# Kernel tuning notes

Hardware: AMD Instinct MI355X
Metric: run time of the kernel (lower is better)

## Reference

```python
import jax, jax.numpy as jnp
import numpy as np
import math

B, S, H, W, C = 8, 16, 512, 512, 1
NT, WIN, SIGMA, ITERS = 256, 21, 2.0, 5
K = WIN * WIN

_SOBEL_X = jnp.array([[-1., 0., 1.], [-2., 0., 2.], [-1., 0., 1.]], jnp.float32).reshape(3, 3, 1, 1)
_SOBEL_Y = jnp.array([[-1., -2., -1.], [0., 0., 0.], [1., 2., 1.]], jnp.float32).reshape(3, 3, 1, 1)


def _win_weights():
    c = WIN // 2
    yy, xx = np.mgrid[0:WIN, 0:WIN]
    d = np.sqrt((xx - c) ** 2 + (yy - c) ** 2)
    g = 1.0 / (SIGMA * math.sqrt(2 * math.pi)) * np.exp(-0.5 * (d / SIGMA) ** 2)
    return jnp.asarray(g.reshape(K), dtype=jnp.float32)


def _sampling_grid():
    lin = jnp.linspace(-1.0, 1.0, WIN)
    x_t, y_t = jnp.meshgrid(lin, lin)  # 'xy' indexing, matches tf.meshgrid
    return jnp.stack([x_t.reshape(-1), y_t.reshape(-1)])  # [2, K]


def _bilinear(sampler, frames2):
    # sampler [B,NT,2,K]; frames2 [B,2,H,W] -> samples [B,2,NT,K]
    x = sampler[:, :, 0] * (WIN * 0.5)  # [B,NT,K] pixel coords
    y = sampler[:, :, 1] * (WIN * 0.5)
    x0 = jnp.clip(jnp.floor(x), 0, W - 1)
    x1 = jnp.clip(jnp.floor(x) + 1, 0, W - 1)
    y0 = jnp.clip(jnp.floor(y), 0, H - 1)
    y1 = jnp.clip(jnp.floor(y) + 1, 0, H - 1)
    wa = (y1 - y) * (x1 - x)
    wb = (y1 - y) * (x - x0)
    wc = (y - y0) * (x1 - x)
    wd = (y - y0) * (x - x0)
    flat = frames2.reshape(frames2.shape[0], 2, H * W)

    def gat(yi, xi):
        idx = (yi.astype(jnp.int32) * W + xi.astype(jnp.int32)).reshape(yi.shape[0], 1, -1)
        idx = jnp.broadcast_to(idx, (yi.shape[0], 2, idx.shape[-1]))
        return jnp.take_along_axis(flat, idx, axis=2).reshape(-1, 2, NT, K)

    Ia, Ib, Ic, Id = gat(y0, x0), gat(y0, x1), gat(y1, x0), gat(y1, x1)
    return (wa[:, None] * Ia + wb[:, None] * Ib + wc[:, None] * Ic + wd[:, None] * Id)


def _calc_velocity(first, second, ww):
    # first/second [B,NT,K] windows; LK 2x2 normal-equation solve per track
    img = first.reshape(-1, WIN, WIN, 1)
    dn = ('NHWC', 'HWIO', 'NHWC')
    Ix = jax.lax.conv_general_dilated(img, _SOBEL_X, (1, 1), 'SAME', dimension_numbers=dn).reshape(-1, NT, K)
    Iy = jax.lax.conv_general_dilated(img, _SOBEL_Y, (1, 1), 'SAME', dimension_numbers=dn).reshape(-1, NT, K)
    A = jnp.stack([Ix, Iy], axis=-1)  # [B,NT,K,2]
    ATA = jnp.einsum('bnki,bnkj->bnij', A, A * ww[None, None, :, None])
    a, b = ATA[..., 0, 0], ATA[..., 0, 1]
    c, d = ATA[..., 1, 0], ATA[..., 1, 1]
    inv_det = 1.0 / (a * d - b * c + 1e-7)
    bvec = -(second - first) * ww  # [B,NT,K]
    ATb = jnp.einsum('bnki,bnk->bni', A, bvec)
    vx = inv_det * (d * ATb[..., 0] - b * ATb[..., 1])
    vy = inv_det * (-c * ATb[..., 0] + a * ATb[..., 1])
    return jnp.stack([vx, vy], axis=-1)  # [B,NT,2]


def _iterative_lk(sampler, frames2, ww):
    out = _bilinear(sampler, frames2)
    first = out[:, 0]
    v = _calc_velocity(first, out[:, 1], ww)
    sampler = sampler + v[..., None]
    sum_v = v
    for _ in range(ITERS - 1):
        out = _bilinear(sampler, frames2)
        v = _calc_velocity(first, out[:, 1], ww)
        sampler = sampler + v[..., None]
        sum_v = sum_v + v
    return sampler, sum_v


def setup_inputs() -> dict:
    key = jax.random.key(0)
    k1, k2 = jax.random.split(key)
    track_locs = jax.random.uniform(k1, (B, NT, 2), dtype=jnp.float32)
    imgs = jax.random.uniform(k2, (B, S, H, W, C), dtype=jnp.float32)
    return {"track_locs": track_locs, "imgs": imgs}


def reference(track_locs, imgs):
    imgs2 = imgs[..., 0]  # [B,S,H,W], c==1
    cr = jnp.array([W / WIN, H / WIN], jnp.float32)
    ww = _win_weights()
    init = track_locs.reshape(-1, NT, 2) * cr + cr  # [B,NT,2]
    sampler = init[..., None] + _sampling_grid()[None, None]  # [B,NT,2,K]
    sampler, sv = _iterative_lk(sampler, imgs2[:, 0:2], ww)
    pos0 = init
    pos1 = init + sv
    fa = jnp.moveaxis(imgs2[:, 1:S - 1], 1, 0)  # [S-2,B,H,W]
    fb = jnp.moveaxis(imgs2[:, 2:S], 1, 0)

    def step(carry, x):
        smp, prev = carry
        frames2 = jnp.stack(x, axis=1)  # [B,2,H,W]
        smp, svv = _iterative_lk(smp, frames2, ww)
        pos = prev + svv
        return (smp, pos), pos

    _, poss = jax.lax.scan(step, (sampler, pos1), (fa, fb))
    tot = jnp.concatenate([pos0[None], pos1[None], poss], axis=0)  # [S,B,NT,2]
    tot = jnp.transpose(tot, (1, 2, 0, 3))  # [B,NT,S,2]
    return (tot - cr) / cr
```

## Files before the change

### kernel.cpp

```cpp
#pragma clang fp contract(off)
#include <hip/hip_runtime.h>
#include <math.h>


#define WINSZ 21
#define KPTS  441
#define NPT   7
#define PSTR  452
#define RDIM  24
#define RSTR  25

struct SB {
  float pqT[6][PSTR];
  float fw[23][25];
  float regA[RDIM * RSTR];
  float regB[RDIM * RSTR];
};

__device__ __forceinline__ float bilinf(const float* __restrict__ F,
                                        float x, float y) {
  #pragma clang fp contract(off)
  float fx = floorf(x), fy = floorf(y);
  float x0 = fminf(fmaxf(fx, 0.0f), 511.0f);
  float x1a = fx + 1.0f;
  float x1 = fminf(fmaxf(x1a, 0.0f), 511.0f);
  float y0 = fminf(fmaxf(fy, 0.0f), 511.0f);
  float y1a = fy + 1.0f;
  float y1 = fminf(fmaxf(y1a, 0.0f), 511.0f);
  float dy1 = y1 - y, dx1 = x1 - x, dy0 = y - y0, dx0 = x - x0;
  float wa = dy1 * dx1;
  float wb = dy1 * dx0;
  float wc = dy0 * dx1;
  float wd = dy0 * dx0;
  int jx0 = (int)x0, jx1 = (int)x1, jy0 = (int)y0, jy1 = (int)y1;
  float Ia = F[jy0 * 512 + jx0];
  float Ib = F[jy0 * 512 + jx1];
  float Ic = F[jy1 * 512 + jx0];
  float Id = F[jy1 * 512 + jx1];
  float pA = wa * Ia;
  float pB = wb * Ib;
  float pC = wc * Ic;
  float pD = wd * Id;
  float s = pA + pB;
  s = s + pC;
  s = s + pD;
  return s;
}

__device__ __forceinline__ void wcalc(float x, float y, int cb,
                                      float* w, int* idx) {
  #pragma clang fp contract(off)
  float fx = floorf(x), fy = floorf(y);
  float x1 = fx + 1.0f;
  float y1 = fy + 1.0f;
  float dy1 = y1 - y, dx1 = x1 - x, dy0 = y - fy, dx0 = x - fx;
  w[0] = dy1 * dx1;
  w[1] = dy1 * dx0;
  w[2] = dy0 * dx1;
  w[3] = dy0 * dx0;
  int ix0 = (int)fx, iy0 = (int)fy;
  *idx = iy0 * RSTR + ix0 - cb;
}

__device__ __forceinline__ float rsum(const float* __restrict__ reg,
                                      const float* w, int idx) {
  #pragma clang fp contract(off)
  float Ia = reg[idx];
  float Ib = reg[idx + 1];
  float Ic = reg[idx + RSTR];
  float Id = reg[idx + RSTR + 1];
  float pA = w[0] * Ia;
  float pB = w[1] * Ib;
  float pC = w[2] * Ic;
  float pD = w[3] * Id;
  float s = pA + pB;
  s = s + pC;
  s = s + pD;
  return s;
}

__global__ __launch_bounds__(64) void lk_track(
    const float* __restrict__ track_locs,
    const float* __restrict__ imgs,
    float* __restrict__ out)
{
  #pragma clang fp contract(off)
  __shared__ SB S;
  const float CRF = (float)(512.0 / 21.0);
  const int SS = 16, HW = 512 * 512;

  const int tr   = blockIdx.x;
  const int b    = tr >> 8;
  const int lane = threadIdx.x;

  for (int i = lane; i < 23 * 25; i += 64) (&S.fw[0][0])[i] = 0.0f;

  const bool act = (lane < 63);
  int   rr[NPT], cc[NPT];
  float gxv[NPT], gyv[NPT], wwv[NPT];
  const double gnorm = 1.0 / (2.0 * sqrt(2.0 * 3.141592653589793));
#pragma unroll
  for (int j = 0; j < NPT; j++) {
    int k = lane * NPT + j;
    if (k >= KPTS) k = 0;
    int r = k / WINSZ, c = k % WINSZ;
    rr[j] = r; cc[j] = c;
    gxv[j] = (c == 20) ? 1.0f : (float)((double)c * 0.1 - 1.0);
    gyv[j] = (r == 20) ? 1.0f : (float)((double)r * 0.1 - 1.0);
    double dd = sqrt((double)((c - 10) * (c - 10) + (r - 10) * (r - 10)));
    double q  = dd / 2.0;
    wwv[j] = (float)(gnorm * exp(-0.5 * (q * q)));
  }

  int soff[9], loff[9];
#pragma unroll
  for (int i = 0; i < 9; i++) {
    int f = lane + 64 * i;
    int r = f / RDIM;
    int c = f - RDIM * r;
    soff[i] = r * 512 + c;
    loff[i] = r * RSTR + c;
  }

  const float* tl = track_locs + (size_t)tr * 2;
  float mx = tl[0] * CRF; float initx = mx + CRF;
  float my = tl[1] * CRF; float inity = my + CRF;

  float sx[NPT], sy[NPT];
#pragma unroll
  for (int j = 0; j < NPT; j++) { sx[j] = initx + gxv[j]; sy[j] = inity + gyv[j]; }

  float px = initx, py = inity;
  if (lane == 0) {
    float* o = out + (size_t)tr * SS * 2;
    float n0 = initx - CRF; o[0] = n0 / CRF;
    float n1 = inity - CRF; o[1] = n1 / CRF;
  }

  int g6 = lane >> 3; if (g6 > 5) g6 = g6 - 2;
  const int grp2 = lane >> 5;
  const float* row6 = &S.pqT[g6][0];
  const float* rowB = &S.pqT[4 + grp2][0];

  float fv[NPT], scv[NPT], ixv[NPT], iyv[NPT];

  for (int t = 0; t < SS - 1; t++) {
    const float* F0 = imgs + ((size_t)b * SS + t) * HW;
    const float* F1 = F0 + HW;

    __syncthreads();

    float xmn = sx[0], xmx = sx[0], ymn = sy[0], ymx = sy[0];
#pragma unroll
    for (int j = 1; j < NPT; j++) {
      xmn = fminf(xmn, sx[j]); xmx = fmaxf(xmx, sx[j]);
      ymn = fminf(ymn, sy[j]); ymx = fmaxf(ymx, sy[j]);
    }
#pragma unroll
    for (int m = 32; m >= 1; m >>= 1) {
      xmn = fminf(xmn, __shfl_xor(xmn, m, 64));
      xmx = fmaxf(xmx, __shfl_xor(xmx, m, 64));
      ymn = fminf(ymn, __shfl_xor(ymn, m, 64));
      ymx = fmaxf(ymx, __shfl_xor(ymx, m, 64));
    }
    float xminp = xmn * 10.5f, xmaxp = xmx * 10.5f;
    float yminp = ymn * 10.5f, ymaxp = ymx * 10.5f;
    float bxf = floorf(xminp), byf = floorf(yminp);
    bool fast = (bxf >= 0.0f) && (byf >= 0.0f) &&
                (bxf <= 488.0f) && (byf <= 488.0f) &&
                (xmaxp < bxf + 23.0f) && (ymaxp < byf + 23.0f);
    int gbase = 0, cb = 0;
    if (fast) {
      int bx = (int)bxf, by = (int)byf;
      gbase = by * 512 + bx;
      cb = by * RSTR + bx;
    }

    if (fast) {
#pragma unroll
      for (int i = 0; i < 9; i++) S.regA[loff[i]] = F0[gbase + soff[i]];
#pragma unroll
      for (int i = 0; i < 9; i++) S.regB[loff[i]] = F1[gbase + soff[i]];
      __syncthreads();
#pragma unroll
      for (int j = 0; j < NPT; j++) {
        float x = sx[j] * 10.5f, y = sy[j] * 10.5f;
        float w[4]; int id;
        wcalc(x, y, cb, w, &id);
        fv[j]  = rsum(S.regA, w, id);
        scv[j] = rsum(S.regB, w, id);
        if (act) S.fw[rr[j] + 1][cc[j] + 1] = fv[j];
      }
    } else {
#pragma unroll
      for (int j = 0; j < NPT; j++) {
        float x = sx[j] * 10.5f, y = sy[j] * 10.5f;
        fv[j]  = bilinf(F0, x, y);
        scv[j] = bilinf(F1, x, y);
        if (act) S.fw[rr[j] + 1][cc[j] + 1] = fv[j];
      }
    }
    __syncthreads();

#pragma unroll
    for (int j = 0; j < NPT; j++) {
      int r = rr[j], c = cc[j];
      float a00 = S.fw[r][c],     a01 = S.fw[r][c + 1],     a02 = S.fw[r][c + 2];
      float a10 = S.fw[r + 1][c],                           a12 = S.fw[r + 1][c + 2];
      float a20 = S.fw[r + 2][c], a21 = S.fw[r + 2][c + 1], a22 = S.fw[r + 2][c + 2];
      float xc0 = -a00;
      float xc1 = 2.0f * a12;
      float xc2 = a02 + (-a20);
      float xc3 = -2.0f * a10;
      float xh0 = xc0 + xc1;
      float xh1 = xc2 + xc3;
      float Ix = xh0 + xh1;
      Ix = Ix + a22;
      float yc0 = -a00;
      float yc1 = -2.0f * a01;
      float yc2 = (-a02) + a20;
      float yc3 = 2.0f * a21;
      float yh0 = yc0 + yc1;
      float yh1 = yc2 + yc3;
      float Iy = yh0 + yh1;
      Iy = Iy + a22;
      ixv[j] = Ix; iyv[j] = Iy;
      if (act) {
        int k = lane * NPT + j;
        float tx = Ix * wwv[j];
        float ty = Iy * wwv[j];
        float p0 = Ix * tx;
        float p1 = Ix * ty;
        float p2 = Iy * tx;
        float p3 = Iy * ty;
        S.pqT[0][k] = p0;
        S.pqT[1][k] = p1;
        S.pqT[2][k] = p2;
        S.pqT[3][k] = p3;
        float d2 = fv[j] - scv[j];
        float bw = d2 * wwv[j];
        float u0 = ixv[j] * bw;
        float u1 = iyv[j] * bw;
        S.pqT[4][k] = u0;
        S.pqT[5][k] = u1;
      }
    }
    __syncthreads();

    float acc = 0.f;
#pragma unroll 11
    for (int m = 0; m < 110; m++) {
      float4 v = *reinterpret_cast<const float4*>(&row6[4 * m]);
      acc = acc + v.x;
      acc = acc + v.y;
      acc = acc + v.z;
      acc = acc + v.w;
    }
    acc = acc + row6[440];
    float aa = __shfl(acc, 0,  64);
    float bb = __shfl(acc, 8,  64);
    float cN = __shfl(acc, 16, 64);
    float dN = __shfl(acc, 24, 64);
    float s0 = __shfl(acc, 32, 64);
    float s1 = __shfl(acc, 40, 64);
    float q0 = aa * dN;
    float q1 = bb * cN;
    float det = q0 - q1;
    det = det + 1e-7f;
    float inv_det = 1.0f / det;

    float svx = 0.f, svy = 0.f;
    for (int it = 0; it < 5; it++) {
      if (it > 0) {
        float xmn2 = sx[0], xmx2 = sx[0], ymn2 = sy[0], ymx2 = sy[0];
#pragma unroll
        for (int j = 1; j < NPT; j++) {
          xmn2 = fminf(xmn2, sx[j]); xmx2 = fmaxf(xmx2, sx[j]);
          ymn2 = fminf(ymn2, sy[j]); ymx2 = fmaxf(ymx2, sy[j]);
        }
#pragma unroll
        for (int m = 32; m >= 1; m >>= 1) {
          xmn2 = fminf(xmn2, __shfl_xor(xmn2, m, 64));
          xmx2 = fmaxf(xmx2, __shfl_xor(xmx2, m, 64));
          ymn2 = fminf(ymn2, __shfl_xor(ymn2, m, 64));
          ymx2 = fmaxf(ymx2, __shfl_xor(ymx2, m, 64));
        }
        float xminp2 = xmn2 * 10.5f, xmaxp2 = xmx2 * 10.5f;
        float yminp2 = ymn2 * 10.5f, ymaxp2 = ymx2 * 10.5f;
        float bxf2 = floorf(xminp2), byf2 = floorf(yminp2);
        bool fast2 = (bxf2 >= 0.0f) && (byf2 >= 0.0f) &&
                     (bxf2 <= 488.0f) && (byf2 <= 488.0f) &&
                     (xmaxp2 < bxf2 + 23.0f) && (ymaxp2 < byf2 + 23.0f);
        if (fast2) {
          int bx2 = (int)bxf2, by2 = (int)byf2;
          int gbase2 = by2 * 512 + bx2;
          int cb2 = by2 * RSTR + bx2;
#pragma unroll
          for (int i = 0; i < 9; i++) S.regB[loff[i]] = F1[gbase2 + soff[i]];
          __syncthreads();
#pragma unroll
          for (int j = 0; j < NPT; j++) {
            float x = sx[j] * 10.5f, y = sy[j] * 10.5f;
            float w[4]; int id;
            wcalc(x, y, cb2, w, &id);
            scv[j] = rsum(S.regB, w, id);
          }
        } else {
#pragma unroll
          for (int j = 0; j < NPT; j++) {
            float x = sx[j] * 10.5f, y = sy[j] * 10.5f;
            scv[j] = bilinf(F1, x, y);
          }
        }
#pragma unroll
        for (int j = 0; j < NPT; j++) {
          if (act) {
            int k = lane * NPT + j;
            float d2 = fv[j] - scv[j];
            float bw = d2 * wwv[j];
            float u0 = ixv[j] * bw;
            float u1 = iyv[j] * bw;
            S.pqT[4][k] = u0;
            S.pqT[5][k] = u1;
          }
        }
        __syncthreads();
        float accB = 0.f;
#pragma unroll 11
        for (int m = 0; m < 110; m++) {
          float4 v = *reinterpret_cast<const float4*>(&rowB[4 * m]);
          accB = accB + v.x;
          accB = accB + v.y;
          accB = accB + v.z;
          accB = accB + v.w;
        }
        accB = accB + rowB[440];
        s0 = __shfl(accB, 0,  64);
        s1 = __shfl(accB, 32, 64);
      }
      float e0 = dN * s0;
      float e1 = bb * s1;
      float numx = e0 - e1;
      float vx = inv_det * numx;
      float f0 = (-cN) * s0;
      float f1 = aa * s1;
      float numy = f0 + f1;
      float vy = inv_det * numy;
#pragma unroll
      for (int j = 0; j < NPT; j++) { sx[j] = sx[j] + vx; sy[j] = sy[j] + vy; }
      if (it == 0) { svx = vx;       svy = vy; }
      else         { svx = svx + vx; svy = svy + vy; }
      __syncthreads();
    }

    px = px + svx; py = py + svy;
    if (lane == 0) {
      float* o = out + ((size_t)tr * SS + (t + 1)) * 2;
      float n0 = px - CRF; o[0] = n0 / CRF;
      float n1 = py - CRF; o[1] = n1 / CRF;
    }
  }
}

extern "C" void kernel_launch(void* const* d_in, const int* in_sizes, int n_in,
                              void* d_out, int out_size, void* d_ws, size_t ws_size,
                              hipStream_t stream) {
  const float* tl   = (const float*)d_in[0];
  const float* imgs = (const float*)d_in[1];
  float* o          = (float*)d_out;
  lk_track<<<dim3(2048), dim3(64), 0, stream>>>(tl, imgs, o);
}
```

Measured before the change: 334.0 us.

## Enlarge LDS image patch with margin and reuse it across iterations and frames

```diff
diff --git a/kernel.cpp b/kernel.cpp
--- a/kernel.cpp
+++ b/kernel.cpp
@@ -7,14 +7,16 @@
 #define KPTS  441
 #define NPT   7
 #define PSTR  452
-#define RDIM  24
-#define RSTR  25
+#define RDIM  26
+#define RSTR  27
+#define RPXN  676
+#define REPS  0.03125f
 
 struct SB {
   float pqT[6][PSTR];
   float fw[23][25];
-  float regA[RDIM * RSTR];
-  float regB[RDIM * RSTR];
+  float reg0[RDIM * RSTR];
+  float reg1[RDIM * RSTR];
 };
 
 __device__ __forceinline__ float bilinf(const float* __restrict__ F,
@@ -112,10 +114,11 @@
     wwv[j] = (float)(gnorm * exp(-0.5 * (q * q)));
   }
 
-  int soff[9], loff[9];
-#pragma unroll
-  for (int i = 0; i < 9; i++) {
+  int soff[11], loff[11];
+#pragma unroll
+  for (int i = 0; i < 11; i++) {
     int f = lane + 64 * i;
+    if (f >= RPXN) f = 0;
     int r = f / RDIM;
     int c = f - RDIM * r;
     soff[i] = r * 512 + c;
@@ -142,6 +145,11 @@
   const float* row6 = &S.pqT[g6][0];
   const float* rowB = &S.pqT[4 + grp2][0];
 
+  float* rPrev = &S.reg0[0];
+  bool  havePrev = false;
+  float bxPf = 0.f, byPf = 0.f;
+  int   cbPrev = 0;
+
   float fv[NPT], scv[NPT], ixv[NPT], iyv[NPT];
 
   for (int t = 0; t < SS - 1; t++) {
@@ -150,55 +158,75 @@
 
     __syncthreads();
 
-    float xmn = sx[0], xmx = sx[0], ymn = sy[0], ymx = sy[0];
-#pragma unroll
-    for (int j = 1; j < NPT; j++) {
-      xmn = fminf(xmn, sx[j]); xmx = fmaxf(xmx, sx[j]);
-      ymn = fminf(ymn, sy[j]); ymx = fmaxf(ymx, sy[j]);
-    }
-#pragma unroll
-    for (int m = 32; m >= 1; m >>= 1) {
-      xmn = fminf(xmn, __shfl_xor(xmn, m, 64));
-      xmx = fmaxf(xmx, __shfl_xor(xmx, m, 64));
-      ymn = fminf(ymn, __shfl_xor(ymn, m, 64));
-      ymx = fmaxf(ymx, __shfl_xor(ymx, m, 64));
-    }
-    float xminp = xmn * 10.5f, xmaxp = xmx * 10.5f;
-    float yminp = ymn * 10.5f, ymaxp = ymx * 10.5f;
-    float bxf = floorf(xminp), byf = floorf(yminp);
-    bool fast = (bxf >= 0.0f) && (byf >= 0.0f) &&
-                (bxf <= 488.0f) && (byf <= 488.0f) &&
-                (xmaxp < bxf + 23.0f) && (ymaxp < byf + 23.0f);
-    int gbase = 0, cb = 0;
-    if (fast) {
+    float s0x = __shfl(sx[0], 0, 64);
+    float s0y = __shfl(sy[0], 0, 64);
+    float xminp = (s0x - REPS) * 10.5f;
+    float xmaxp = (s0x + (2.0f + REPS)) * 10.5f;
+    float yminp = (s0y - REPS) * 10.5f;
+    float ymaxp = (s0y + (2.0f + REPS)) * 10.5f;
+    float bxf = floorf(xminp) - 1.0f;
+    float byf = floorf(yminp) - 1.0f;
+    bool inb = (bxf >= 0.0f) && (byf >= 0.0f) &&
+               (bxf <= 486.0f) && (byf <= 486.0f) &&
+               (xmaxp < bxf + 25.0f) && (ymaxp < byf + 25.0f);
+    bool reuseA = havePrev &&
+                  (xminp >= bxPf) && (xmaxp < bxPf + 25.0f) &&
+                  (yminp >= byPf) && (ymaxp < byPf + 25.0f);
+
+    float* rA; float* rB;
+    if (reuseA) {
+      rA = rPrev;
+      rB = (rPrev == &S.reg0[0]) ? &S.reg1[0] : &S.reg0[0];
+    } else {
+      rA = &S.reg0[0];
+      rB = &S.reg1[0];
+    }
+    int cbA = 0, cbB = 0;
+    bool fastA = false, haveB = false;
+    float bxBf = 0.f, byBf = 0.f;
+    if (inb) {
       int bx = (int)bxf, by = (int)byf;
-      gbase = by * 512 + bx;
-      cb = by * RSTR + bx;
-    }
-
-    if (fast) {
-#pragma unroll
-      for (int i = 0; i < 9; i++) S.regA[loff[i]] = F0[gbase + soff[i]];
-#pragma unroll
-      for (int i = 0; i < 9; i++) S.regB[loff[i]] = F1[gbase + soff[i]];
+      int gbase = by * 512 + bx;
+      int cbN = by * RSTR + bx;
+      if (!reuseA) {
+#pragma unroll
+        for (int i = 0; i < 11; i++) {
+          int f = lane + 64 * i;
+          if (f < RPXN) rA[loff[i]] = F0[gbase + soff[i]];
+        }
+        cbA = cbN;
+      } else cbA = cbPrev;
+#pragma unroll
+      for (int i = 0; i < 11; i++) {
+        int f = lane + 64 * i;
+        if (f < RPXN) rB[loff[i]] = F1[gbase + soff[i]];
+      }
+      cbB = cbN; bxBf = bxf; byBf = byf;
+      fastA = true; haveB = true;
       __syncthreads();
-#pragma unroll
-      for (int j = 0; j < NPT; j++) {
-        float x = sx[j] * 10.5f, y = sy[j] * 10.5f;
+    } else if (reuseA) {
+      cbA = cbPrev;
+      fastA = true;
+    }
+
+#pragma unroll
+    for (int j = 0; j < NPT; j++) {
+      float x = sx[j] * 10.5f, y = sy[j] * 10.5f;
+      if (fastA) {
         float w[4]; int id;
-        wcalc(x, y, cb, w, &id);
-        fv[j]  = rsum(S.regA, w, id);
-        scv[j] = rsum(S.regB, w, id);
-        if (act) S.fw[rr[j] + 1][cc[j] + 1] = fv[j];
-      }
-    } else {
-#pragma unroll
-      for (int j = 0; j < NPT; j++) {
-        float x = sx[j] * 10.5f, y = sy[j] * 10.5f;
+        wcalc(x, y, cbA, w, &id);
+        fv[j] = rsum(rA, w, id);
+        if (haveB) {
+          int idb = id + (cbA - cbB);
+          scv[j] = rsum(rB, w, idb);
+        } else {
+          scv[j] = bilinf(F1, x, y);
+        }
+      } else {
         fv[j]  = bilinf(F0, x, y);
         scv[j] = bilinf(F1, x, y);
-        if (act) S.fw[rr[j] + 1][cc[j] + 1] = fv[j];
       }
+      if (act) S.fw[rr[j] + 1][cc[j] + 1] = fv[j];
     }
     __syncthreads();
 
@@ -272,43 +300,45 @@
     float svx = 0.f, svy = 0.f;
     for (int it = 0; it < 5; it++) {
       if (it > 0) {
-        float xmn2 = sx[0], xmx2 = sx[0], ymn2 = sy[0], ymx2 = sy[0];
-#pragma unroll
-        for (int j = 1; j < NPT; j++) {
-          xmn2 = fminf(xmn2, sx[j]); xmx2 = fmaxf(xmx2, sx[j]);
-          ymn2 = fminf(ymn2, sy[j]); ymx2 = fmaxf(ymx2, sy[j]);
-        }
-#pragma unroll
-        for (int m = 32; m >= 1; m >>= 1) {
-          xmn2 = fminf(xmn2, __shfl_xor(xmn2, m, 64));
-          xmx2 = fmaxf(xmx2, __shfl_xor(xmx2, m, 64));
-          ymn2 = fminf(ymn2, __shfl_xor(ymn2, m, 64));
-          ymx2 = fmaxf(ymx2, __shfl_xor(ymx2, m, 64));
-        }
-        float xminp2 = xmn2 * 10.5f, xmaxp2 = xmx2 * 10.5f;
-        float yminp2 = ymn2 * 10.5f, ymaxp2 = ymx2 * 10.5f;
-        float bxf2 = floorf(xminp2), byf2 = floorf(yminp2);
-        bool fast2 = (bxf2 >= 0.0f) && (byf2 >= 0.0f) &&
-                     (bxf2 <= 488.0f) && (byf2 <= 488.0f) &&
-                     (xmaxp2 < bxf2 + 23.0f) && (ymaxp2 < byf2 + 23.0f);
-        if (fast2) {
-          int bx2 = (int)bxf2, by2 = (int)byf2;
-          int gbase2 = by2 * 512 + bx2;
-          int cb2 = by2 * RSTR + bx2;
-#pragma unroll
-          for (int i = 0; i < 9; i++) S.regB[loff[i]] = F1[gbase2 + soff[i]];
-          __syncthreads();
-#pragma unroll
-          for (int j = 0; j < NPT; j++) {
-            float x = sx[j] * 10.5f, y = sy[j] * 10.5f;
+        float t0x = __shfl(sx[0], 0, 64);
+        float t0y = __shfl(sy[0], 0, 64);
+        float xminp2 = (t0x - REPS) * 10.5f;
+        float xmaxp2 = (t0x + (2.0f + REPS)) * 10.5f;
+        float yminp2 = (t0y - REPS) * 10.5f;
+        float ymaxp2 = (t0y + (2.0f + REPS)) * 10.5f;
+        bool reuseB = haveB &&
+                      (xminp2 >= bxBf) && (xmaxp2 < bxBf + 25.0f) &&
+                      (yminp2 >= byBf) && (ymaxp2 < byBf + 25.0f);
+        if (!reuseB) {
+          float bxf2 = floorf(xminp2) - 1.0f;
+          float byf2 = floorf(yminp2) - 1.0f;
+          bool inb2 = (bxf2 >= 0.0f) && (byf2 >= 0.0f) &&
+                      (bxf2 <= 486.0f) && (byf2 <= 486.0f) &&
+                      (xmaxp2 < bxf2 + 25.0f) && (ymaxp2 < byf2 + 25.0f);
+          if (inb2) {
+            int bx2 = (int)bxf2, by2 = (int)byf2;
+            int gbase2 = by2 * 512 + bx2;
+#pragma unroll
+            for (int i = 0; i < 11; i++) {
+              int f = lane + 64 * i;
+              if (f < RPXN) rB[loff[i]] = F1[gbase2 + soff[i]];
+            }
+            cbB = by2 * RSTR + bx2;
+            bxBf = bxf2; byBf = byf2;
+            haveB = true;
+            __syncthreads();
+          } else {
+            haveB = false;
+          }
+        }
+#pragma unroll
+        for (int j = 0; j < NPT; j++) {
+          float x = sx[j] * 10.5f, y = sy[j] * 10.5f;
+          if (haveB) {
             float w[4]; int id;
-            wcalc(x, y, cb2, w, &id);
-            scv[j] = rsum(S.regB, w, id);
-          }
-        } else {
-#pragma unroll
-          for (int j = 0; j < NPT; j++) {
-            float x = sx[j] * 10.5f, y = sy[j] * 10.5f;
+            wcalc(x, y, cbB, w, &id);
+            scv[j] = rsum(rB, w, id);
+          } else {
             scv[j] = bilinf(F1, x, y);
           }
         }
@@ -353,6 +383,10 @@
       __syncthreads();
     }
 
+    rPrev = rB;
+    havePrev = haveB;
+    bxPf = bxBf; byPf = byBf; cbPrev = cbB;
+
     px = px + svx; py = py + svy;
     if (lane == 0) {
       float* o = out + ((size_t)tr * SS + (t + 1)) * 2;
```

Result: no change. 335.7 us (+0.5%).
